# Kernel optimization log

Measured on AMD Instinct MI355X. Metric: run time of the kernel, lower is better.

## Reference

```python
import jax, jax.numpy as jnp
import numpy as np
from functools import partial

VOCAB, EMB = 32000, 512
HIDDEN = (1024, 512, 256)
OUT = 7
S, T = 1024, 64  # S = scan (seq) axis, T = 'timesteps' (effective batch)


def _lstm_layer(x, Wih, Whh, bih, bhh):
    """PyTorch-semantics LSTM over axis 0. x: (S, B, E) -> hs: (S, B, H)."""
    B = x.shape[1]
    H = Whh.shape[1]
    # precompute input contribution to all gates: (S, B, 4H)
    xg = jnp.einsum('sbe,ge->sbg', x, Wih) + bih + bhh

    def step(carry, xg_t):
        h, c = carry
        gates = xg_t + h @ Whh.T  # (B, 4H)
        i, f, g, o = jnp.split(gates, 4, axis=-1)  # torch gate order i,f,g,o
        i = jax.nn.sigmoid(i)
        f = jax.nn.sigmoid(f)
        g = jnp.tanh(g)
        o = jax.nn.sigmoid(o)
        c = f * c + i * g
        h = o * jnp.tanh(c)
        return (h, c), h

    init = (jnp.zeros((B, H), x.dtype), jnp.zeros((B, H), x.dtype))
    _, hs = jax.lax.scan(step, init, xg)
    return hs


def setup_inputs():
    key = jax.random.key(0)
    ks = jax.random.split(key, 16)
    inp = {
        'tokens': jax.random.randint(ks[0], (S, T), 0, VOCAB),
        'emb': jax.random.normal(ks[1], (VOCAB, EMB), jnp.float32) * 0.02,
    }
    dims = [(EMB, HIDDEN[0]), (HIDDEN[0], HIDDEN[1]), (HIDDEN[1], HIDDEN[2])]
    for li, (e, h) in enumerate(dims):
        s = 1.0 / np.sqrt(h)
        inp[f'Wih{li}'] = jax.random.uniform(ks[2 + 4 * li], (4 * h, e), jnp.float32, -s, s)
        inp[f'Whh{li}'] = jax.random.uniform(ks[3 + 4 * li], (4 * h, h), jnp.float32, -s, s)
        inp[f'bih{li}'] = jax.random.uniform(ks[4 + 4 * li], (4 * h,), jnp.float32, -s, s)
        inp[f'bhh{li}'] = jax.random.uniform(ks[5 + 4 * li], (4 * h,), jnp.float32, -s, s)
    s = 1.0 / np.sqrt(HIDDEN[2])
    inp['Wlin'] = jax.random.uniform(ks[14], (OUT, HIDDEN[2]), jnp.float32, -s, s)
    inp['blin'] = jax.random.uniform(ks[15], (OUT,), jnp.float32, -s, s)
    return inp


def reference(tokens, emb, Wih0, Whh0, bih0, bhh0, Wih1, Whh1, bih1, bhh1,
              Wih2, Whh2, bih2, bhh2, Wlin, blin):
    x = emb[tokens]                                  # (S, T, EMB)
    h = _lstm_layer(x, Wih0, Whh0, bih0, bhh0)       # (S, T, 1024)
    h = _lstm_layer(h, Wih1, Whh1, bih1, bhh1)       # (S, T, 512)
    h = _lstm_layer(h, Wih2, Whh2, bih2, bhh2)       # (S, T, 256)
    last = h[:, T - 1, :]                            # out[:, timesteps-1, :]
    out = last @ Wlin.T + blin                       # (S, OUT); dropout is identity in eval
    return out
```

## Files before the change

kernel.cpp:

```cpp
#include <hip/hip_runtime.h>
#include <math.h>

#define SLEN 1024

__device__ __forceinline__ float sigf(float x) { return 1.0f / (1.0f + __expf(-x)); }

__device__ __forceinline__ float agent_ld(const float* p) {
  return __hip_atomic_load(p, __ATOMIC_RELAXED, __HIP_MEMORY_SCOPE_AGENT);
}
__device__ __forceinline__ void agent_st(float* p, float v) {
  __hip_atomic_store(p, v, __ATOMIC_RELAXED, __HIP_MEMORY_SCOPE_AGENT);
}
__device__ __forceinline__ bool is_sent(float f) { return __float_as_uint(f) == 0xFFFFFFFFu; }

__device__ __forceinline__ void pin4(float4& v) {
  asm volatile("" : "+v"(v.x), "+v"(v.y), "+v"(v.z), "+v"(v.w));
}
#define DOT4(acc, wv, iv)                                                  \
  acc += (wv).x * (iv).x + (wv).y * (iv).y + (wv).z * (iv).z + (wv).w * (iv).w

__global__ __launch_bounds__(512, 2) void xg0_k(const int* __restrict__ tokens,
                                                const float* __restrict__ emb,
                                                const float* __restrict__ Wih0,
                                                const float* __restrict__ bih0,
                                                const float* __restrict__ bhh0,
                                                float* __restrict__ xg0) {
  const int tid = threadIdx.x, c = tid & 63, w = tid >> 6;
  const int ublk = blockIdx.x & 127;
  const int tpar = blockIdx.x >> 7;
  const int u = ublk * 8 + w;
  const float4* emb4 = (const float4*)emb;
  float4 wr[4][2];
  float bb[4];
  #pragma unroll
  for (int g = 0; g < 4; ++g) {
    const size_t row = (size_t)g * 1024 + u;
    const float4* w4 = (const float4*)(Wih0 + row * 512);
    wr[g][0] = w4[2 * c];
    wr[g][1] = w4[2 * c + 1];
    bb[g] = bih0[row] + bhh0[row];
  }
  float4* xg4 = (float4*)xg0;
  for (int t = tpar; t < SLEN; t += 2) {
    const int tok = tokens[t * 64 + 63];
    const float4 e0 = emb4[(size_t)tok * 128 + 2 * c];
    const float4 e1 = emb4[(size_t)tok * 128 + 2 * c + 1];
    float a[4] = {0.f, 0.f, 0.f, 0.f};
    #pragma unroll
    for (int g = 0; g < 4; ++g) { DOT4(a[g], wr[g][0], e0); DOT4(a[g], wr[g][1], e1); }
    #pragma unroll
    for (int off = 32; off > 0; off >>= 1)
      #pragma unroll
      for (int g = 0; g < 4; ++g) a[g] += __shfl_xor(a[g], off);
    if (c == 0)
      xg4[(size_t)t * 1024 + u] =
          make_float4(a[0] + bb[0], a[1] + bb[1], a[2] + bb[2], a[3] + bb[3]);
  }
}

__device__ void l0_role(int ublk, const float* __restrict__ Whh,
                        const float* __restrict__ xg0, float* __restrict__ hout) {
  __shared__ __align__(16) float in_lds[2][1024];
  __shared__ float h_g[8];
  const int tid = threadIdx.x, c = tid & 63, w = tid >> 6;
  const int u0 = ublk * 8, u = u0 + w;

  float4 wreg[4][4];
  #pragma unroll
  for (int g = 0; g < 4; ++g) {
    const float4* whh4 = (const float4*)(Whh + ((size_t)g * 1024 + u) * 1024);
    #pragma unroll
    for (int s = 0; s < 4; ++s) wreg[g][s] = whh4[s * 64 + c];
  }
  const float4* xg4 = (const float4*)xg0;
  float cst = 0.f;

  for (int t = 0; t < SLEN; ++t) {
    #pragma unroll
    for (int g = 0; g < 4; ++g)
      #pragma unroll
      for (int s = 0; s < 4; ++s) pin4(wreg[g][s]);

    float4 xgv = make_float4(0.f, 0.f, 0.f, 0.f);
    if (c == 0) xgv = xg4[(size_t)t * 1024 + u];

    float hv0 = 0.f, hv1 = 0.f;
    if (t > 0) {
      const float* hsrc = hout + (size_t)(t - 1) * 1024 + 2 * tid;
      for (;;) {
        hv0 = agent_ld(hsrc);
        hv1 = agent_ld(hsrc + 1);
        if (!is_sent(hv0) && !is_sent(hv1)) break;
        __builtin_amdgcn_s_sleep(1);
      }
    }
    float* dst = in_lds[t & 1];
    dst[2 * tid] = hv0;
    dst[2 * tid + 1] = hv1;
    __syncthreads();

    float a[4] = {0.f, 0.f, 0.f, 0.f};
    const float4* iv4 = (const float4*)dst;
    #pragma unroll
    for (int s = 0; s < 4; ++s) {
      const float4 iv = iv4[s * 64 + c];
      #pragma unroll
      for (int g = 0; g < 4; ++g) DOT4(a[g], wreg[g][s], iv);
    }
    #pragma unroll
    for (int off = 32; off > 0; off >>= 1)
      #pragma unroll
      for (int g = 0; g < 4; ++g) a[g] += __shfl_xor(a[g], off);

    if (c == 0) {
      const float I = sigf(a[0] + xgv.x);
      const float F = sigf(a[1] + xgv.y);
      const float G = tanhf(a[2] + xgv.z);
      const float O = sigf(a[3] + xgv.w);
      cst = F * cst + I * G;
      h_g[w] = O * tanhf(cst);
    }
    __syncthreads();
    if (tid < 8) agent_st(hout + (size_t)t * 1024 + u0 + tid, h_g[tid]);
  }
}

template<int HOUT, int EIN>
__device__ void lstm_role(int ublk,
                          const float* __restrict__ Wih, const float* __restrict__ Whh,
                          const float* __restrict__ bih, const float* __restrict__ bhh,
                          const float* __restrict__ in_hist, float* __restrict__ hout) {
  constexpr int C     = EIN + HOUT;
  constexpr int SLOTS = C / 256;
  constexpr int XQ    = EIN / 4;
  constexpr int EPN   = EIN / 512;
  constexpr int HPN   = 1;
  constexpr bool HGUARD = (HOUT < 512);

  __shared__ __align__(16) float in_lds[2][C];
  __shared__ float h_g[8];

  const int tid = threadIdx.x, c = tid & 63, w = tid >> 6;
  const int u0 = ublk * 8, u = u0 + w;

  float4 wreg[4][SLOTS];
  #pragma unroll
  for (int g = 0; g < 4; ++g) {
    const size_t grow = (size_t)g * HOUT + (size_t)u;
    const float4* wih4 = (const float4*)(Wih + grow * EIN);
    const float4* whh4 = (const float4*)(Whh + grow * HOUT);
    #pragma unroll
    for (int s = 0; s < SLOTS; ++s) {
      const int c4 = s * 64 + c;
      wreg[g][s] = (c4 < XQ) ? wih4[c4] : whh4[c4 - XQ];
    }
  }
  float bg[4] = {0.f, 0.f, 0.f, 0.f};
  float cst = 0.f;
  if (c == 0) {
    #pragma unroll
    for (int g = 0; g < 4; ++g) bg[g] = bih[g * HOUT + u] + bhh[g * HOUT + u];
  }

  for (int t = 0; t < SLEN; ++t) {
    #pragma unroll
    for (int g = 0; g < 4; ++g)
      #pragma unroll
      for (int s = 0; s < SLOTS; ++s) pin4(wreg[g][s]);

    float ev[EPN];
    float hv = 0.f;
    const float* esrc = in_hist + (size_t)t * EIN + EPN * tid;
    const float* hsrc = hout + (size_t)((t > 0 ? t : 1) - 1) * HOUT + tid;
    const bool hon   = (!HGUARD) || (tid < HOUT);
    const bool hneed = (t > 0) && hon;

    for (;;) {
      bool ok = true;
      #pragma unroll
      for (int i = 0; i < EPN; ++i) ev[i] = agent_ld(esrc + i);
      if (hneed) { hv = agent_ld(hsrc); ok &= !is_sent(hv); }
      #pragma unroll
      for (int i = 0; i < EPN; ++i) ok &= !is_sent(ev[i]);
      if (ok) break;
      __builtin_amdgcn_s_sleep(1);
    }
    if (!hneed) hv = 0.f;

    float* dst = in_lds[t & 1];
    #pragma unroll
    for (int i = 0; i < EPN; ++i) dst[EPN * tid + i] = ev[i];
    if (hon) dst[EIN + tid] = hv;
    __syncthreads();

    float a[4] = {0.f, 0.f, 0.f, 0.f};
    const float4* iv4 = (const float4*)dst;
    #pragma unroll
    for (int s = 0; s < SLOTS; ++s) {
      const float4 iv = iv4[s * 64 + c];
      #pragma unroll
      for (int g = 0; g < 4; ++g) DOT4(a[g], wreg[g][s], iv);
    }
    #pragma unroll
    for (int off = 32; off > 0; off >>= 1)
      #pragma unroll
      for (int g = 0; g < 4; ++g) a[g] += __shfl_xor(a[g], off);

    if (c == 0) {
      const float I = sigf(a[0] + bg[0]);
      const float F = sigf(a[1] + bg[1]);
      const float G = tanhf(a[2] + bg[2]);
      const float O = sigf(a[3] + bg[3]);
      cst = F * cst + I * G;
      h_g[w] = O * tanhf(cst);
    }
    __syncthreads();
    if (tid < 8) agent_st(hout + (size_t)t * HOUT + u0 + tid, h_g[tid]);
  }
}

__device__ void final_role(int fb, const float* __restrict__ h2,
                           const float* __restrict__ Wlin, const float* __restrict__ blin,
                           float* __restrict__ out) {
  const int tid = threadIdx.x;
  float wl[7];
  #pragma unroll
  for (int o = 0; o < 7; ++o) wl[o] = 0.f;
  if (tid < 256) {
    #pragma unroll
    for (int o = 0; o < 7; ++o) wl[o] = Wlin[o * 256 + tid];
  }
  __shared__ float red[4][7];
  for (int t = fb; t < SLEN; t += 8) {
    float h = 0.0f;
    if (tid < 256) {
      h = agent_ld(h2 + (size_t)t * 256 + tid);
      while (is_sent(h)) {
        __builtin_amdgcn_s_sleep(1);
        h = agent_ld(h2 + (size_t)t * 256 + tid);
      }
    }
    float p[7];
    #pragma unroll
    for (int o = 0; o < 7; ++o) p[o] = h * wl[o];
    #pragma unroll
    for (int off = 32; off > 0; off >>= 1) {
      #pragma unroll
      for (int o = 0; o < 7; ++o) p[o] += __shfl_xor(p[o], off);
    }
    const int w = tid >> 6;
    if (w < 4 && (tid & 63) == 0) {
      #pragma unroll
      for (int o = 0; o < 7; ++o) red[w][o] = p[o];
    }
    __syncthreads();
    if (tid == 0) {
      #pragma unroll
      for (int o = 0; o < 7; ++o)
        out[t * 7 + o] = red[0][o] + red[1][o] + red[2][o] + red[3][o] + blin[o];
    }
    __syncthreads();
  }
}

__global__ __attribute__((amdgpu_flat_work_group_size(512, 512),
                          amdgpu_waves_per_eu(2, 2))) void pipe_k(
    const float* __restrict__ xg0,
    const float* __restrict__ Whh0,
    const float* __restrict__ Wih1, const float* __restrict__ Whh1,
    const float* __restrict__ bih1, const float* __restrict__ bhh1,
    const float* __restrict__ Wih2, const float* __restrict__ Whh2,
    const float* __restrict__ bih2, const float* __restrict__ bhh2,
    const float* __restrict__ Wlin, const float* __restrict__ blin,
    float* __restrict__ h0, float* __restrict__ h1, float* __restrict__ h2,
    float* __restrict__ out) {
  const int b = blockIdx.x;
  if (b < 128) {
    l0_role(b, Whh0, xg0, h0);
  } else if (b < 192) {
    lstm_role<512, 1024>(b - 128, Wih1, Whh1, bih1, bhh1, h0, h1);
  } else if (b < 224) {
    lstm_role<256, 512>(b - 192, Wih2, Whh2, bih2, bhh2, h1, h2);
  } else {
    final_role(b - 224, h2, Wlin, blin, out);
  }
}

extern "C" void kernel_launch(void* const* d_in, const int* in_sizes, int n_in,
                              void* d_out, int out_size, void* d_ws, size_t ws_size,
                              hipStream_t stream) {
  const int*   tokens = (const int*)  d_in[0];
  const float* emb  = (const float*)d_in[1];
  const float* Wih0 = (const float*)d_in[2];
  const float* Whh0 = (const float*)d_in[3];
  const float* bih0 = (const float*)d_in[4];
  const float* bhh0 = (const float*)d_in[5];
  const float* Wih1 = (const float*)d_in[6];
  const float* Whh1 = (const float*)d_in[7];
  const float* bih1 = (const float*)d_in[8];
  const float* bhh1 = (const float*)d_in[9];
  const float* Wih2 = (const float*)d_in[10];
  const float* Whh2 = (const float*)d_in[11];
  const float* bih2 = (const float*)d_in[12];
  const float* bhh2 = (const float*)d_in[13];
  const float* Wlin = (const float*)d_in[14];
  const float* blin = (const float*)d_in[15];

  float* xg0 = (float*)d_ws;
  float* h0  = xg0 + (size_t)1024 * 4096;
  float* h1  = h0 + (size_t)1024 * 1024;
  float* h2  = h1 + (size_t)1024 * 512;

  hipMemsetAsync(h0, 0xFF,
                 ((size_t)1024 * 1024 + (size_t)1024 * 512 + (size_t)1024 * 256) *
                     sizeof(float),
                 stream);
  xg0_k<<<256, 512, 0, stream>>>(tokens, emb, Wih0, bih0, bhh0, xg0);
  pipe_k<<<232, 512, 0, stream>>>(xg0, Whh0,
                                  Wih1, Whh1, bih1, bhh1,
                                  Wih2, Whh2, bih2, bhh2,
                                  Wlin, blin, h0, h1, h2, (float*)d_out);
}
```

Baseline: 3.100 ms.

## Spill part of layer-1/2 weights to LDS, drop spin sleeps, widen xg0 grid

Layers 1 and 2 now keep only three weight slots per gate in registers; the remaining slots are staged once into a large dynamic LDS blob and read from LDS every step. This cuts register pressure that likely caused spills for the layer-1 role with six slots. The spin-wait loops no longer call s_sleep, which shortens the wake-up latency between pipeline stages at the cost of more polling traffic. The xg0 precompute kernel uses four times as many blocks for more parallelism. The large dynamic LDS allocation may limit how many blocks can be resident per CU.

```diff
diff --git a/kernel.cpp b/kernel.cpp
--- a/kernel.cpp
+++ b/kernel.cpp
@@ -27,7 +27,7 @@
                                                 float* __restrict__ xg0) {
   const int tid = threadIdx.x, c = tid & 63, w = tid >> 6;
   const int ublk = blockIdx.x & 127;
-  const int tpar = blockIdx.x >> 7;
+  const int tph  = blockIdx.x >> 7;
   const int u = ublk * 8 + w;
   const float4* emb4 = (const float4*)emb;
   float4 wr[4][2];
@@ -41,7 +41,7 @@
     bb[g] = bih0[row] + bhh0[row];
   }
   float4* xg4 = (float4*)xg0;
-  for (int t = tpar; t < SLEN; t += 2) {
+  for (int t = tph; t < SLEN; t += 8) {
     const int tok = tokens[t * 64 + 63];
     const float4 e0 = emb4[(size_t)tok * 128 + 2 * c];
     const float4 e1 = emb4[(size_t)tok * 128 + 2 * c + 1];
@@ -58,10 +58,10 @@
   }
 }
 
-__device__ void l0_role(int ublk, const float* __restrict__ Whh,
+__device__ void l0_role(int ublk, char* blob, const float* __restrict__ Whh,
                         const float* __restrict__ xg0, float* __restrict__ hout) {
-  __shared__ __align__(16) float in_lds[2][1024];
-  __shared__ float h_g[8];
+  float* in_base = (float*)blob;
+  float* hg = in_base + 2 * 1024;
   const int tid = threadIdx.x, c = tid & 63, w = tid >> 6;
   const int u0 = ublk * 8, u = u0 + w;
 
@@ -91,10 +91,9 @@
         hv0 = agent_ld(hsrc);
         hv1 = agent_ld(hsrc + 1);
         if (!is_sent(hv0) && !is_sent(hv1)) break;
-        __builtin_amdgcn_s_sleep(1);
       }
     }
-    float* dst = in_lds[t & 1];
+    float* dst = in_base + (t & 1) * 1024;
     dst[2 * tid] = hv0;
     dst[2 * tid + 1] = hv1;
     __syncthreads();
@@ -118,39 +117,50 @@
       const float G = tanhf(a[2] + xgv.z);
       const float O = sigf(a[3] + xgv.w);
       cst = F * cst + I * G;
-      h_g[w] = O * tanhf(cst);
-    }
-    __syncthreads();
-    if (tid < 8) agent_st(hout + (size_t)t * 1024 + u0 + tid, h_g[tid]);
-  }
-}
-
-template<int HOUT, int EIN>
-__device__ void lstm_role(int ublk,
+      hg[w] = O * tanhf(cst);
+    }
+    __syncthreads();
+    if (tid < 8) agent_st(hout + (size_t)t * 1024 + u0 + tid, hg[tid]);
+  }
+}
+
+template<int HOUT, int EIN, int RSLOTS>
+__device__ void lstm_role(int ublk, char* blob,
                           const float* __restrict__ Wih, const float* __restrict__ Whh,
                           const float* __restrict__ bih, const float* __restrict__ bhh,
                           const float* __restrict__ in_hist, float* __restrict__ hout) {
-  constexpr int C     = EIN + HOUT;
-  constexpr int SLOTS = C / 256;
-  constexpr int XQ    = EIN / 4;
-  constexpr int EPN   = EIN / 512;
-  constexpr int HPN   = 1;
+  constexpr int C      = EIN + HOUT;
+  constexpr int SLOTS  = C / 256;
+  constexpr int LSLOTS = SLOTS - RSLOTS;
+  constexpr int XQ     = EIN / 4;
+  constexpr int EPN    = EIN / 512;
   constexpr bool HGUARD = (HOUT < 512);
 
-  __shared__ __align__(16) float in_lds[2][C];
-  __shared__ float h_g[8];
+  float4* wlds4  = (float4*)blob;
+  float* in_base = (float*)blob + (size_t)LSLOTS * 32 * 64 * 4;
+  float* hg      = in_base + 2 * C;
 
   const int tid = threadIdx.x, c = tid & 63, w = tid >> 6;
   const int u0 = ublk * 8, u = u0 + w;
 
-  float4 wreg[4][SLOTS];
+  for (int k = tid; k < LSLOTS * 32 * 64; k += 512) {
+    const int cc = k & 63, rr = k >> 6, r = rr & 31, sl = rr >> 5;
+    const int g = r & 3, wu = r >> 2;
+    const size_t grow = (size_t)g * HOUT + (size_t)(u0 + wu);
+    const float4* wih4 = (const float4*)(Wih + grow * EIN);
+    const float4* whh4 = (const float4*)(Whh + grow * HOUT);
+    const int c4 = (RSLOTS + sl) * 64 + cc;
+    wlds4[k] = (c4 < XQ) ? wih4[c4] : whh4[c4 - XQ];
+  }
+
+  float4 wreg[4][RSLOTS];
   #pragma unroll
   for (int g = 0; g < 4; ++g) {
     const size_t grow = (size_t)g * HOUT + (size_t)u;
     const float4* wih4 = (const float4*)(Wih + grow * EIN);
     const float4* whh4 = (const float4*)(Whh + grow * HOUT);
     #pragma unroll
-    for (int s = 0; s < SLOTS; ++s) {
+    for (int s = 0; s < RSLOTS; ++s) {
       const int c4 = s * 64 + c;
       wreg[g][s] = (c4 < XQ) ? wih4[c4] : whh4[c4 - XQ];
     }
@@ -166,7 +176,7 @@
     #pragma unroll
     for (int g = 0; g < 4; ++g)
       #pragma unroll
-      for (int s = 0; s < SLOTS; ++s) pin4(wreg[g][s]);
+      for (int s = 0; s < RSLOTS; ++s) pin4(wreg[g][s]);
 
     float ev[EPN];
     float hv = 0.f;
@@ -183,11 +193,10 @@
       #pragma unroll
       for (int i = 0; i < EPN; ++i) ok &= !is_sent(ev[i]);
       if (ok) break;
-      __builtin_amdgcn_s_sleep(1);
     }
     if (!hneed) hv = 0.f;
 
-    float* dst = in_lds[t & 1];
+    float* dst = in_base + (t & 1) * C;
     #pragma unroll
     for (int i = 0; i < EPN; ++i) dst[EPN * tid + i] = ev[i];
     if (hon) dst[EIN + tid] = hv;
@@ -196,10 +205,19 @@
     float a[4] = {0.f, 0.f, 0.f, 0.f};
     const float4* iv4 = (const float4*)dst;
     #pragma unroll
-    for (int s = 0; s < SLOTS; ++s) {
+    for (int s = 0; s < RSLOTS; ++s) {
       const float4 iv = iv4[s * 64 + c];
       #pragma unroll
       for (int g = 0; g < 4; ++g) DOT4(a[g], wreg[g][s], iv);
+    }
+    #pragma unroll
+    for (int sl = 0; sl < LSLOTS; ++sl) {
+      const float4 iv = iv4[(RSLOTS + sl) * 64 + c];
+      #pragma unroll
+      for (int g = 0; g < 4; ++g) {
+        const float4 wv = wlds4[((sl * 32) + (w * 4 + g)) * 64 + c];
+        DOT4(a[g], wv, iv);
+      }
     }
     #pragma unroll
     for (int off = 32; off > 0; off >>= 1)
@@ -212,10 +230,10 @@
       const float G = tanhf(a[2] + bg[2]);
       const float O = sigf(a[3] + bg[3]);
       cst = F * cst + I * G;
-      h_g[w] = O * tanhf(cst);
-    }
-    __syncthreads();
-    if (tid < 8) agent_st(hout + (size_t)t * HOUT + u0 + tid, h_g[tid]);
+      hg[w] = O * tanhf(cst);
+    }
+    __syncthreads();
+    if (tid < 8) agent_st(hout + (size_t)t * HOUT + u0 + tid, hg[tid]);
   }
 }
 
@@ -235,10 +253,7 @@
     float h = 0.0f;
     if (tid < 256) {
       h = agent_ld(h2 + (size_t)t * 256 + tid);
-      while (is_sent(h)) {
-        __builtin_amdgcn_s_sleep(1);
-        h = agent_ld(h2 + (size_t)t * 256 + tid);
-      }
+      while (is_sent(h)) h = agent_ld(h2 + (size_t)t * 256 + tid);
     }
     float p[7];
     #pragma unroll
@@ -262,6 +277,8 @@
     __syncthreads();
   }
 }
+
+#define PIPE_DYN_LDS 110624
 
 __global__ __attribute__((amdgpu_flat_work_group_size(512, 512),
                           amdgpu_waves_per_eu(2, 2))) void pipe_k(
@@ -274,13 +291,15 @@
     const float* __restrict__ Wlin, const float* __restrict__ blin,
     float* __restrict__ h0, float* __restrict__ h1, float* __restrict__ h2,
     float* __restrict__ out) {
+  extern __shared__ float4 dyn4[];
+  char* blob = (char*)dyn4;
   const int b = blockIdx.x;
   if (b < 128) {
-    l0_role(b, Whh0, xg0, h0);
+    l0_role(b, blob, Whh0, xg0, h0);
   } else if (b < 192) {
-    lstm_role<512, 1024>(b - 128, Wih1, Whh1, bih1, bhh1, h0, h1);
+    lstm_role<512, 1024, 3>(b - 128, blob, Wih1, Whh1, bih1, bhh1, h0, h1);
   } else if (b < 224) {
-    lstm_role<256, 512>(b - 192, Wih2, Whh2, bih2, bhh2, h1, h2);
+    lstm_role<256, 512, 3>(b - 192, blob, Wih2, Whh2, bih2, bhh2, h1, h2);
   } else {
     final_role(b - 224, h2, Wlin, blin, out);
   }
@@ -311,13 +330,17 @@
   float* h1  = h0 + (size_t)1024 * 1024;
   float* h2  = h1 + (size_t)1024 * 512;
 
+  (void)hipFuncSetAttribute((const void*)pipe_k,
+                            hipFuncAttributeMaxDynamicSharedMemorySize,
+                            PIPE_DYN_LDS);
+
   hipMemsetAsync(h0, 0xFF,
                  ((size_t)1024 * 1024 + (size_t)1024 * 512 + (size_t)1024 * 256) *
                      sizeof(float),
                  stream);
-  xg0_k<<<256, 512, 0, stream>>>(tokens, emb, Wih0, bih0, bhh0, xg0);
-  pipe_k<<<232, 512, 0, stream>>>(xg0, Whh0,
-                                  Wih1, Whh1, bih1, bhh1,
-                                  Wih2, Whh2, bih2, bhh2,
-                                  Wlin, blin, h0, h1, h2, (float*)d_out);
-}
+  xg0_k<<<1024, 512, 0, stream>>>(tokens, emb, Wih0, bih0, bhh0, xg0);
+  pipe_k<<<232, 512, PIPE_DYN_LDS, stream>>>(xg0, Whh0,
+                                             Wih1, Whh1, bih1, bhh1,
+                                             Wih2, Whh2, bih2, bhh2,
+                                             Wlin, blin, h0, h1, h2, (float*)d_out);
+}
```

New measurement: 2.947 ms. -4.9%, faster.
